# Optimization experiments

Hardware: AMD Instinct MI355X
Metric: run time of the kernel (lower is better)

The kernel has to match this reference:

```python
import jax, jax.numpy as jnp
import numpy as np

N_EXP, N_DICT, N_PIX = 2048, 65536, 1600

def setup_inputs() -> dict:
    key = jax.random.key(0)
    k1, k2, k3 = jax.random.split(key, 3)
    return {
        "experimental_data": jax.random.normal(k1, (N_EXP, N_PIX), dtype=jnp.float32),
        "patterns": jax.random.normal(k2, (N_DICT, N_PIX), dtype=jnp.float32),
        "so3_samples_fz": jax.random.normal(k3, (N_DICT, 4), dtype=jnp.float32),
        "topk": 10,
    }

def reference(experimental_data, patterns, so3_samples_fz, topk):
    # di_patterns: subtract per-pattern mean from experimental data
    q = experimental_data - jnp.mean(experimental_data, axis=1, keepdims=True)
    # _project_dictionary: dictionary patterns are mean-subtracted at projection time
    d = patterns - jnp.mean(patterns, axis=1, keepdims=True)
    # angular distance metric: normalize, dot, arccos; min angle == max cosine
    qn = q * jax.lax.rsqrt(jnp.sum(q * q, axis=1, keepdims=True))
    dn = d * jax.lax.rsqrt(jnp.sum(d * d, axis=1, keepdims=True))
    cos_sim = jnp.einsum("qp,dp->qd", qn, dn)            # [n_exp, n_dict]
    top_cos, top_idx = jax.lax.top_k(cos_sim, topk)       # [n_exp, topk]
    top_ang = jnp.arccos(jnp.clip(top_cos, -1.0, 1.0))    # angular distance of matches
    # lookup_orientations: gather matched quaternions from the SO(3) FZ sampling
    orientations = so3_samples_fz[top_idx]                # [n_exp, topk, 4]
    return top_ang, top_idx, orientations
```

## Files before the change

### kernel.cpp

```cpp
#include <hip/hip_runtime.h>
#include <stdint.h>

#define N_EXP  2048
#define N_DICT 65536
#define N_PIX  1600
#define TOPK   10
#define K1     16
#define KTH    8
#define K2     16
#define NBLK   512
#define NCAND  (NBLK * 4)

#define BM 128
#define BN 128
#define BK 64
#define KTILES (N_PIX / BK)

typedef __attribute__((ext_vector_type(8))) __bf16 bf16x8;
typedef __attribute__((ext_vector_type(4))) float  f32x4;

__device__ __forceinline__ unsigned short f2bf(float f) {
    unsigned int u = __float_as_uint(f);
    unsigned int r = (u + 0x7FFFu + ((u >> 16) & 1u)) >> 16;
    return (unsigned short)r;
}

__device__ __forceinline__ float sel4f(const float a[4], int p) {
    return p == 0 ? a[0] : (p == 1 ? a[1] : (p == 2 ? a[2] : a[3]));
}
__device__ __forceinline__ int sel4i(const int a[4], int p) {
    return p == 0 ? a[0] : (p == 1 ? a[1] : (p == 2 ? a[2] : a[3]));
}

__device__ __forceinline__ float blockReduceSumF(float v) {
    __shared__ float p[4];
    #pragma unroll
    for (int o = 32; o > 0; o >>= 1) v += __shfl_down(v, o);
    __syncthreads();
    if ((threadIdx.x & 63) == 0) p[threadIdx.x >> 6] = v;
    __syncthreads();
    return p[0] + p[1] + p[2] + p[3];
}

__global__ __launch_bounds__(256) void prep_rows(const float* __restrict__ in,
                                                 unsigned short* __restrict__ outb) {
    const int row = blockIdx.x;
    const int tid = threadIdx.x;
    const float* x = in + (size_t)row * N_PIX;
    float v[7];
    float s = 0.f;
    #pragma unroll
    for (int it = 0; it < 7; ++it) {
        int j = tid + it * 256;
        float t = (j < N_PIX) ? x[j] : 0.f;
        v[it] = t; s += t;
    }
    s = blockReduceSumF(s);
    const float mean = s * (1.0f / N_PIX);
    float ss = 0.f;
    #pragma unroll
    for (int it = 0; it < 7; ++it) {
        int j = tid + it * 256;
        float c = v[it] - mean;
        if (j < N_PIX) ss += c * c;
    }
    ss = blockReduceSumF(ss);
    const float rn = rsqrtf(ss);
    unsigned short* o = outb + (size_t)row * N_PIX;
    #pragma unroll
    for (int it = 0; it < 7; ++it) {
        int j = tid + it * 256;
        if (j < N_PIX) o[j] = f2bf((v[it] - mean) * rn);
    }
}

__global__ __launch_bounds__(256) void gemm_topk(const unsigned short* __restrict__ A,
                                                 const unsigned short* __restrict__ B,
                                                 float* __restrict__ cand_s,
                                                 int* __restrict__ cand_i) {
    __shared__ __attribute__((aligned(16))) char smem[32768];
    unsigned short* As = (unsigned short*)smem;
    unsigned short* Bs = (unsigned short*)(smem + 16384);
    float*          Ss = (float*)smem;

    const int tid  = threadIdx.x;
    const int lane = tid & 63;
    const int w    = tid >> 6;
    const int wm   = w >> 1, wn = w & 1;

    const int id  = blockIdx.x;
    const int xcd = id & 7;
    const int j_  = id >> 3;
    const int bm  = j_ & 15;
    const int bn  = (j_ >> 4) * 8 + xcd;

    const unsigned short* Ag = A + (size_t)bm * BM * N_PIX;
    const unsigned short* Bg = B + (size_t)bn * BN * N_PIX;

    const int ldr = lane >> 3;
    const int ldc = (((lane & 7) ^ ldr) * 8);
    const int m    = lane & 15;
    const int quad = lane >> 4;

    f32x4 acc[4][4];
    #pragma unroll
    for (int i = 0; i < 4; ++i)
        #pragma unroll
        for (int j = 0; j < 4; ++j)
            acc[i][j] = (f32x4){0.f, 0.f, 0.f, 0.f};

    for (int kt = 0; kt < KTILES; ++kt) {
        const int k0 = kt * BK;
        #pragma unroll
        for (int t = 0; t < 4; ++t) {
            int r = w * 32 + t * 8 + ldr;
            __builtin_amdgcn_global_load_lds(
                (const __attribute__((address_space(1))) void*)(const void*)(Ag + (size_t)r * N_PIX + k0 + ldc),
                (__attribute__((address_space(3))) void*)(void*)((char*)As + (w * 4 + t) * 1024),
                16, 0, 0);
            __builtin_amdgcn_global_load_lds(
                (const __attribute__((address_space(1))) void*)(const void*)(Bg + (size_t)r * N_PIX + k0 + ldc),
                (__attribute__((address_space(3))) void*)(void*)((char*)Bs + (w * 4 + t) * 1024),
                16, 0, 0);
        }
        __syncthreads();
        #pragma unroll
        for (int ks = 0; ks < BK; ks += 32) {
            bf16x8 af[4], bfr[4];
            const int kc = (ks >> 3) + quad;
            const int sw = (kc ^ (m & 7)) * 8;
            #pragma unroll
            for (int i = 0; i < 4; ++i)
                af[i] = *(const bf16x8*)(&As[(wm * 64 + i * 16 + m) * BK + sw]);
            #pragma unroll
            for (int j = 0; j < 4; ++j)
                bfr[j] = *(const bf16x8*)(&Bs[(wn * 64 + j * 16 + m) * BK + sw]);
            #pragma unroll
            for (int i = 0; i < 4; ++i)
                #pragma unroll
                for (int j = 0; j < 4; ++j)
                    acc[i][j] = __builtin_amdgcn_mfma_f32_16x16x32_bf16(af[i], bfr[j], acc[i][j], 0, 0, 0);
        }
        __syncthreads();
    }

    const int row4 = tid >> 2;
    const int part = tid & 3;

    #pragma unroll
    for (int half = 0; half < 2; ++half) {
        __syncthreads();
        if (wm == half) {
            #pragma unroll
            for (int i = 0; i < 4; ++i)
                #pragma unroll
                for (int r = 0; r < 4; ++r) {
                    int row = i * 16 + quad * 4 + r;
                    #pragma unroll
                    for (int j = 0; j < 4; ++j) {
                        int col = wn * 64 + j * 16 + m;
                        Ss[row * 128 + ((col + row) & 127)] = acc[i][j][r];
                    }
                }
        }
        __syncthreads();
        float bs4[4]; int bi4[4];
        bs4[0] = bs4[1] = bs4[2] = bs4[3] = -2.0f;
        bi4[0] = bi4[1] = bi4[2] = bi4[3] = 0;
        #pragma unroll
        for (int k = 0; k < 32; ++k) {
            int col = part * 32 + ((k + 8 * part) & 31);
            float v = Ss[row4 * 128 + ((col + row4) & 127)];
            if (v > bs4[3]) {
                int cix = bn * 128 + col;
                #pragma unroll
                for (int t = 0; t < 4; ++t) {
                    bool sw = v > bs4[t];
                    float ts = bs4[t]; int ti = bi4[t];
                    bs4[t] = sw ? v : ts;  bi4[t] = sw ? cix : ti;
                    v = sw ? ts : v;       cix = sw ? ti : cix;
                }
            }
        }
        #pragma unroll
        for (int s = 1; s <= 2; s <<= 1) {
            float ov[4]; int oi[4];
            #pragma unroll
            for (int t = 0; t < 4; ++t) {
                ov[t] = __shfl_xor(bs4[t], s);
                oi[t] = __shfl_xor(bi4[t], s);
            }
            float rv[4]; int ri[4]; int pa = 0, pb = 0;
            #pragma unroll
            for (int t = 0; t < 4; ++t) {
                float va = sel4f(bs4, pa), vb = sel4f(ov, pb);
                bool ta = (va >= vb);
                rv[t] = ta ? va : vb;
                ri[t] = ta ? sel4i(bi4, pa) : sel4i(oi, pb);
                pa += ta ? 1 : 0; pb += ta ? 0 : 1;
            }
            #pragma unroll
            for (int t = 0; t < 4; ++t) { bs4[t] = rv[t]; bi4[t] = ri[t]; }
        }
        if (part == 0) {
            int grow = bm * BM + half * 64 + row4;
            *(float4*)(cand_s + (size_t)grow * NCAND + bn * 4) =
                make_float4(bs4[0], bs4[1], bs4[2], bs4[3]);
            *(int4*)(cand_i + (size_t)grow * NCAND + bn * 4) =
                make_int4(bi4[0], bi4[1], bi4[2], bi4[3]);
        }
    }
}

__global__ __launch_bounds__(256) void merge_cands(const float* __restrict__ cand_s,
                                                   const int* __restrict__ cand_i,
                                                   int* __restrict__ sel_g) {
    __shared__ float Ms[256 * K1];
    __shared__ int   Mi[256 * K1];
    const int row = blockIdx.x, tid = threadIdx.x;
    const float* s = cand_s + (size_t)row * NCAND;
    const int*   x = cand_i + (size_t)row * NCAND;

    float ls[KTH]; int li[KTH];
    #pragma unroll
    for (int t = 0; t < KTH; ++t) { ls[t] = -2.f; li[t] = 0; }
    #pragma unroll
    for (int it = 0; it < NCAND / 256; ++it) {
        int j = tid + it * 256;
        float v = s[j];
        if (v > ls[KTH - 1]) {
            float cv = v; int ci = x[j];
            #pragma unroll
            for (int t = 0; t < KTH; ++t) {
                bool sw = cv > ls[t];
                float ts = ls[t]; int ti = li[t];
                ls[t] = sw ? cv : ts; li[t] = sw ? ci : ti;
                cv = sw ? ts : cv;   ci = sw ? ti : ci;
            }
        }
    }
    #pragma unroll
    for (int t = 0; t < KTH; ++t) { Ms[tid * K1 + t] = ls[t]; Mi[tid * K1 + t] = li[t]; }
    #pragma unroll
    for (int t = KTH; t < K1; ++t) { Ms[tid * K1 + t] = -3.f; Mi[tid * K1 + t] = 0; }
    __syncthreads();

    #pragma unroll
    for (int lev = 0; lev < 8; ++lev) {
        int stride = 1 << lev;
        if ((tid & (2 * stride - 1)) == 0) {
            int ia = tid * K1, ib = (tid + stride) * K1;
            float rs[K1]; int ri[K1];
            int pa = 0, pb = 0;
            #pragma unroll
            for (int t = 0; t < K1; ++t) {
                float va = Ms[ia + pa], vb = Ms[ib + pb];
                bool ta = (va >= vb);
                rs[t] = ta ? va : vb;
                ri[t] = ta ? Mi[ia + pa] : Mi[ib + pb];
                pa += ta ? 1 : 0; pb += ta ? 0 : 1;
            }
            #pragma unroll
            for (int t = 0; t < K1; ++t) { Ms[ia + t] = rs[t]; Mi[ia + t] = ri[t]; }
        }
        __syncthreads();
    }
    if (tid < K1) sel_g[(size_t)row * K1 + tid] = Mi[tid];
}

__global__ __launch_bounds__(256) void refine_out(const float* __restrict__ expd,
                                                  const float* __restrict__ pat,
                                                  const float* __restrict__ so3,
                                                  const int* __restrict__ sel_g,
                                                  float* __restrict__ out) {
    __shared__ double qc[N_PIX];
    __shared__ double pd[4], pd2[4], pd3[4];
    __shared__ int    sel[K2];
    __shared__ double cosv[K2];
    const int row = blockIdx.x, tid = threadIdx.x;
    const float* x = expd + (size_t)row * N_PIX;

    double s1 = 0.0;
    for (int j = tid; j < N_PIX; j += 256) s1 += (double)x[j];
    #pragma unroll
    for (int o = 32; o > 0; o >>= 1) s1 += __shfl_down(s1, o);
    if ((tid & 63) == 0) pd[tid >> 6] = s1;
    __syncthreads();
    const double mean = (pd[0] + pd[1] + pd[2] + pd[3]) * (1.0 / N_PIX);

    double s2 = 0.0, sc = 0.0;
    for (int j = tid; j < N_PIX; j += 256) {
        double c = (double)x[j] - mean;
        qc[j] = c; s2 += c * c; sc += c;
    }
    #pragma unroll
    for (int o = 32; o > 0; o >>= 1) { s2 += __shfl_down(s2, o); sc += __shfl_down(sc, o); }
    if ((tid & 63) == 0) { pd2[tid >> 6] = s2; pd3[tid >> 6] = sc; }
    if (tid < K2) sel[tid] = sel_g[(size_t)row * K2 + tid];
    __syncthreads();
    const double sumsq = pd2[0] + pd2[1] + pd2[2] + pd2[3];
    const double sqc   = pd3[0] + pd3[1] + pd3[2] + pd3[3];
    const double invq  = 1.0 / sqrt(sumsq);

    const int c  = tid >> 4;
    const int sl = tid & 15;
    const int di = sel[c];
    const float* p = pat + (size_t)di * N_PIX;
    double sp = 0.0, spp = 0.0, sqp = 0.0;
    for (int j = sl; j < N_PIX; j += 16) {
        double pv = (double)p[j];
        sp += pv; spp += pv * pv; sqp += qc[j] * pv;
    }
    #pragma unroll
    for (int o = 8; o > 0; o >>= 1) {
        sp  += __shfl_down(sp,  o, 16);
        spp += __shfl_down(spp, o, 16);
        sqp += __shfl_down(sqp, o, 16);
    }
    if (sl == 0) {
        double mp   = sp * (1.0 / N_PIX);
        double varp = spp - sp * sp * (1.0 / N_PIX);
        double invd = 1.0 / sqrt(varp);
        cosv[c] = (sqp - mp * sqc) * invq * invd;
    }
    __syncthreads();

    if (tid == 0) {
        double cv[K2]; int ci[K2];
        for (int t = 0; t < K2; ++t) { cv[t] = cosv[t]; ci[t] = sel[t]; }
        for (int a = 1; a < K2; ++a) {
            double kv = cv[a]; int ki = ci[a];
            int b = a - 1;
            while (b >= 0 && (cv[b] < kv || (cv[b] == kv && ci[b] > ki))) {
                cv[b + 1] = cv[b]; ci[b + 1] = ci[b]; --b;
            }
            cv[b + 1] = kv; ci[b + 1] = ki;
        }
        float* oa = out;
        float* oi = out + (size_t)N_EXP * TOPK;
        float* oo = out + (size_t)2 * N_EXP * TOPK;
        for (int r = 0; r < TOPK; ++r) {
            double cc = cv[r];
            if (cc > 1.0) cc = 1.0;
            if (cc < -1.0) cc = -1.0;
            oa[(size_t)row * TOPK + r] = (float)acos(cc);
            oi[(size_t)row * TOPK + r] = (float)ci[r];
            int q4 = ci[r];
            #pragma unroll
            for (int t = 0; t < 4; ++t)
                oo[((size_t)row * TOPK + r) * 4 + t] = so3[(size_t)q4 * 4 + t];
        }
    }
}

extern "C" void kernel_launch(void* const* d_in, const int* in_sizes, int n_in,
                              void* d_out, int out_size, void* d_ws, size_t ws_size,
                              hipStream_t stream) {
    const float* expd = (const float*)d_in[0];
    const float* pat  = (const float*)d_in[1];
    const float* so3  = (const float*)d_in[2];
    float* out = (float*)d_out;
    char* ws = (char*)d_ws;

    const size_t QB = (size_t)N_EXP  * N_PIX * 2;
    const size_t DB = (size_t)N_DICT * N_PIX * 2;
    const size_t CB = (size_t)N_EXP  * NCAND * 4;

    unsigned short* Qb = (unsigned short*)ws;
    unsigned short* Db = (unsigned short*)(ws + QB);
    float* cs  = (float*)(ws + QB + DB);
    int*   ci  = (int*)  (ws + QB + DB + CB);
    int*   sel = (int*)  (ws + QB + DB + 2 * CB);

    prep_rows<<<N_EXP, 256, 0, stream>>>(expd, Qb);
    prep_rows<<<N_DICT, 256, 0, stream>>>(pat, Db);
    gemm_topk<<<(N_EXP / BM) * (N_DICT / BN), 256, 0, stream>>>(Qb, Db, cs, ci);
    merge_cands<<<N_EXP, 256, 0, stream>>>(cs, ci, sel);
    refine_out<<<N_EXP, 256, 0, stream>>>(expd, pat, so3, sel, out);
}
```

Baseline: 1.488 ms.

## Enlarge GEMM block tile to 256x128 with 8x4 MFMA accumulators per wave

Doubles the M dimension of the GEMM block tile so each wave computes a 128x64 sub-tile, reusing each loaded B fragment across eight A fragments. Shared memory grows to 48KB and the top-k epilogue now processes four 64-row quarters instead of two halves. This is meant to cut global/LDS traffic per MFMA, at the cost of higher register pressure and lower occupancy.

```diff
diff --git a/kernel.cpp b/kernel.cpp
--- a/kernel.cpp
+++ b/kernel.cpp
@@ -11,7 +11,7 @@
 #define NBLK   512
 #define NCAND  (NBLK * 4)
 
-#define BM 128
+#define BM 256
 #define BN 128
 #define BK 64
 #define KTILES (N_PIX / BK)
@@ -78,9 +78,9 @@
                                                  const unsigned short* __restrict__ B,
                                                  float* __restrict__ cand_s,
                                                  int* __restrict__ cand_i) {
-    __shared__ __attribute__((aligned(16))) char smem[32768];
+    __shared__ __attribute__((aligned(16))) char smem[49152];
     unsigned short* As = (unsigned short*)smem;
-    unsigned short* Bs = (unsigned short*)(smem + 16384);
+    unsigned short* Bs = (unsigned short*)(smem + 32768);
     float*          Ss = (float*)smem;
 
     const int tid  = threadIdx.x;
@@ -91,8 +91,8 @@
     const int id  = blockIdx.x;
     const int xcd = id & 7;
     const int j_  = id >> 3;
-    const int bm  = j_ & 15;
-    const int bn  = (j_ >> 4) * 8 + xcd;
+    const int bm  = j_ & 7;
+    const int bn  = (j_ >> 3) * 8 + xcd;
 
     const unsigned short* Ag = A + (size_t)bm * BM * N_PIX;
     const unsigned short* Bg = B + (size_t)bn * BN * N_PIX;
@@ -102,9 +102,9 @@
     const int m    = lane & 15;
     const int quad = lane >> 4;
 
-    f32x4 acc[4][4];
-    #pragma unroll
-    for (int i = 0; i < 4; ++i)
+    f32x4 acc[8][4];
+    #pragma unroll
+    for (int i = 0; i < 8; ++i)
         #pragma unroll
         for (int j = 0; j < 4; ++j)
             acc[i][j] = (f32x4){0.f, 0.f, 0.f, 0.f};
@@ -112,34 +112,39 @@
     for (int kt = 0; kt < KTILES; ++kt) {
         const int k0 = kt * BK;
         #pragma unroll
-        for (int t = 0; t < 4; ++t) {
-            int r = w * 32 + t * 8 + ldr;
+        for (int t = 0; t < 8; ++t) {
+            int c = w * 8 + t;
+            int r = c * 8 + ldr;
             __builtin_amdgcn_global_load_lds(
                 (const __attribute__((address_space(1))) void*)(const void*)(Ag + (size_t)r * N_PIX + k0 + ldc),
-                (__attribute__((address_space(3))) void*)(void*)((char*)As + (w * 4 + t) * 1024),
+                (__attribute__((address_space(3))) void*)(void*)((char*)As + c * 1024),
                 16, 0, 0);
+        }
+        #pragma unroll
+        for (int t = 0; t < 4; ++t) {
+            int c = w * 4 + t;
+            int r = c * 8 + ldr;
             __builtin_amdgcn_global_load_lds(
                 (const __attribute__((address_space(1))) void*)(const void*)(Bg + (size_t)r * N_PIX + k0 + ldc),
-                (__attribute__((address_space(3))) void*)(void*)((char*)Bs + (w * 4 + t) * 1024),
+                (__attribute__((address_space(3))) void*)(void*)((char*)Bs + c * 1024),
                 16, 0, 0);
         }
         __syncthreads();
         #pragma unroll
         for (int ks = 0; ks < BK; ks += 32) {
-            bf16x8 af[4], bfr[4];
             const int kc = (ks >> 3) + quad;
             const int sw = (kc ^ (m & 7)) * 8;
-            #pragma unroll
-            for (int i = 0; i < 4; ++i)
-                af[i] = *(const bf16x8*)(&As[(wm * 64 + i * 16 + m) * BK + sw]);
+            bf16x8 bfr[4];
             #pragma unroll
             for (int j = 0; j < 4; ++j)
                 bfr[j] = *(const bf16x8*)(&Bs[(wn * 64 + j * 16 + m) * BK + sw]);
             #pragma unroll
-            for (int i = 0; i < 4; ++i)
+            for (int i = 0; i < 8; ++i) {
+                bf16x8 af = *(const bf16x8*)(&As[(wm * 128 + i * 16 + m) * BK + sw]);
                 #pragma unroll
                 for (int j = 0; j < 4; ++j)
-                    acc[i][j] = __builtin_amdgcn_mfma_f32_16x16x32_bf16(af[i], bfr[j], acc[i][j], 0, 0, 0);
+                    acc[i][j] = __builtin_amdgcn_mfma_f32_16x16x32_bf16(af, bfr[j], acc[i][j], 0, 0, 0);
+            }
         }
         __syncthreads();
     }
@@ -148,20 +153,22 @@
     const int part = tid & 3;
 
     #pragma unroll
-    for (int half = 0; half < 2; ++half) {
-        __syncthreads();
-        if (wm == half) {
-            #pragma unroll
-            for (int i = 0; i < 4; ++i)
+    for (int q = 0; q < 4; ++q) {
+        __syncthreads();
+        if (wm == (q >> 1)) {
+            #pragma unroll
+            for (int ii = 0; ii < 4; ++ii) {
+                int i = (q & 1) * 4 + ii;
                 #pragma unroll
                 for (int r = 0; r < 4; ++r) {
-                    int row = i * 16 + quad * 4 + r;
+                    int row = ii * 16 + quad * 4 + r;
                     #pragma unroll
                     for (int j = 0; j < 4; ++j) {
                         int col = wn * 64 + j * 16 + m;
                         Ss[row * 128 + ((col + row) & 127)] = acc[i][j][r];
                     }
                 }
+            }
         }
         __syncthreads();
         float bs4[4]; int bi4[4];
@@ -203,7 +210,7 @@
             for (int t = 0; t < 4; ++t) { bs4[t] = rv[t]; bi4[t] = ri[t]; }
         }
         if (part == 0) {
-            int grow = bm * BM + half * 64 + row4;
+            int grow = bm * BM + q * 64 + row4;
             *(float4*)(cand_s + (size_t)grow * NCAND + bn * 4) =
                 make_float4(bs4[0], bs4[1], bs4[2], bs4[3]);
             *(int4*)(cand_i + (size_t)grow * NCAND + bn * 4) =
```

Result: slower. 1.881 ms (+26.4%).
